# Kernel tuning notes

Hardware: AMD Instinct MI355X
Metric: run time of the kernel (lower is better)

The kernel has to match this reference:

```python
import jax, jax.numpy as jnp
import numpy as np

B, T, D = 32, 512, 1024
P, E, K = 512, 256, 14
NH, L, FF, TOPK = 4, 2, 2048, 7
FOLD_DIV = 2
EPS = 1e-5


def _ln(x, g, b):
    m = x.mean(-1, keepdims=True)
    v = ((x - m) ** 2).mean(-1, keepdims=True)
    return (x - m) * jax.lax.rsqrt(v + EPS) * g + b


def _bn(x, g, b, m, v):  # eval-mode BatchNorm1d with running stats
    return (x - m) * jax.lax.rsqrt(v + EPS) * g + b


def _attn(q, k, v, nh):
    Bq, Tq, Eq = q.shape
    Tk = k.shape[1]
    hd = Eq // nh
    qh = q.reshape(Bq, Tq, nh, hd).transpose(0, 2, 1, 3)
    kh = k.reshape(Bq, Tk, nh, hd).transpose(0, 2, 1, 3)
    vh = v.reshape(Bq, Tk, nh, hd).transpose(0, 2, 1, 3)
    s = jnp.einsum('bhqd,bhkd->bhqk', qh, kh) / jnp.sqrt(jnp.float32(hd))
    a = jax.nn.softmax(s, axis=-1)
    o = jnp.einsum('bhqk,bhkd->bhqd', a, vh)
    return o.transpose(0, 2, 1, 3).reshape(Bq, Tq, Eq)


def setup_inputs() -> dict:
    key = jax.random.key(0)
    ks = iter(jax.random.split(key, 64))

    def rn(shape, s=0.02):
        return jax.random.normal(next(ks), shape, jnp.float32) * s

    return dict(
        x=jax.random.normal(next(ks), (B, T, D), jnp.float32),
        pred_w=rn((D,)), pred_b=jnp.zeros(()),
        t_wqkv=rn((L, D, 3 * D)), t_bqkv=jnp.zeros((L, 3 * D)),
        t_wo=rn((L, D, D)), t_bo=jnp.zeros((L, D)),
        t_ln1g=jnp.ones((L, D)), t_ln1b=jnp.zeros((L, D)),
        t_w1=rn((L, D, FF)), t_b1=jnp.zeros((L, FF)),
        t_w2=rn((L, FF, D)), t_b2=jnp.zeros((L, D)),
        t_ln2g=jnp.ones((L, D)), t_ln2b=jnp.zeros((L, D)),
        sb_w=rn((D, P)), sb_b=jnp.zeros((P,)),
        bn1_g=jnp.ones((P,)), bn1_b=jnp.zeros((P,)), bn1_m=jnp.zeros((P,)), bn1_v=jnp.ones((P,)),
        dt_w=rn((P,)), dt_b=jnp.zeros(()),
        cc_w1=rn((P, 256)), cc_b1=jnp.zeros((256,)),
        bn2_g=jnp.ones((256,)), bn2_b=jnp.zeros((256,)), bn2_m=jnp.zeros((256,)), bn2_v=jnp.ones((256,)),
        cc_w2=rn((256, K)), cc_b2=jnp.zeros((K,)),
        ce=rn((K, E), 1.0),
        kp_w=rn((P, E)), kp_b=jnp.zeros((E,)),
        ca_wqkv=rn((E, 3 * E)), ca_bqkv=jnp.zeros((3 * E,)),
        ca_wo=rn((E, E)), ca_bo=jnp.zeros((E,)),
        fp_w=rn((E, D)), fp_b=jnp.zeros((D,)),
        df_w=rn((P,)), df_b=jnp.zeros(()),
    )


def reference(x, pred_w, pred_b, t_wqkv, t_bqkv, t_wo, t_bo, t_ln1g, t_ln1b, t_w1, t_b1,
              t_w2, t_b2, t_ln2g, t_ln2b, sb_w, sb_b, bn1_g, bn1_b, bn1_m, bn1_v,
              dt_w, dt_b, cc_w1, cc_b1, bn2_g, bn2_b, bn2_m, bn2_v, cc_w2, cc_b2,
              ce, kp_w, kp_b, ca_wqkv, ca_bqkv, ca_wo, ca_bo, fp_w, fp_b, df_w, df_b):
    # --- GlobalAdaptiveTSM: per-token adaptive channel shift, fully vectorized ---
    ratio = jax.nn.sigmoid(jnp.einsum('btd,d->bt', x, pred_w) + pred_b)  # ShiftPredictor
    fold = D // FOLD_DIV
    sn = (ratio * fold).astype(jnp.int32)[..., None]                     # [B,T,1]
    z = jnp.zeros_like(x[:, :1])
    x_prev = jnp.concatenate([z, x[:, :-1]], axis=1)   # t=0 region stays zero
    x_next = jnp.concatenate([x[:, 1:], z], axis=1)    # t=T-1 region stays zero
    c = jnp.arange(D)
    h = jnp.where(c < sn, x_prev, jnp.where(c < 2 * sn, x_next, x))
    # --- TemporalTransformer: 2 post-norm encoder layers (eval mode) ---
    for l in range(L):
        qkv = h @ t_wqkv[l] + t_bqkv[l]
        q, k, v = jnp.split(qkv, 3, axis=-1)
        a = _attn(q, k, v, NH) @ t_wo[l] + t_bo[l]
        h = _ln(h + a, t_ln1g[l], t_ln1b[l])
        f = jax.nn.relu(h @ t_w1[l] + t_b1[l]) @ t_w2[l] + t_b2[l]
        h = _ln(h + f, t_ln2g[l], t_ln2b[l])

    def backbone(zz):
        return jax.nn.relu(_bn(zz @ sb_w + sb_b, bn1_g, bn1_b, bn1_m, bn1_v))

    shared = backbone(h)                                      # [B,T,P]
    top_scores = jnp.einsum('btp,p->bt', shared, dt_w) + dt_b
    _, idx = jax.lax.top_k(top_scores, TOPK)
    agg = jnp.take_along_axis(shared, idx[..., None], axis=1).mean(1)  # [B,P]
    c1 = jax.nn.relu(_bn(agg @ cc_w1 + cc_b1, bn2_g, bn2_b, bn2_m, bn2_v))
    logits = c1 @ cc_w2 + cc_b2                               # [B,K]
    cat_emb = jax.nn.softmax(logits, axis=-1) @ ce            # [B,E]
    proj = shared @ kp_w + kp_b                               # [B,T,E]
    q = cat_emb[:, None, :] @ ca_wqkv[:, :E] + ca_bqkv[:E]
    k = proj @ ca_wqkv[:, E:2 * E] + ca_bqkv[E:2 * E]
    v = proj @ ca_wqkv[:, 2 * E:] + ca_bqkv[2 * E:]
    ctx = _attn(q, k, v, NH) @ ca_wo + ca_bo                  # [B,1,E] broadcasts over T
    final = proj + ctx
    fin_proj = backbone(final @ fp_w + fp_b)
    seg = jnp.einsum('btp,p->bt', fin_proj, df_w) + df_b
    return seg, logits
```

## Files before the change

### kernel.cpp

```cpp
#include <hip/hip_runtime.h>
#include <math.h>

#define Bz 32
#define Tz 512
#define Dz 1024
#define Pz 512
#define Ez 256
#define KC 14
#define NHz 4
#define Lz 2
#define FFz 2048
#define TOPKz 7
#define EPSz 1e-5f
#define BT (Bz*Tz)

typedef unsigned short ushort_t;
typedef __attribute__((ext_vector_type(8))) short short8;
typedef __attribute__((ext_vector_type(4))) float f32x4;

__device__ __forceinline__ ushort_t f2bf(float f) {
    union { float f; unsigned int u; } x; x.f = f;
    unsigned int r = x.u + 0x7fffu + ((x.u >> 16) & 1u);
    return (ushort_t)(r >> 16);
}
__device__ __forceinline__ float bf2f(ushort_t h) {
    union { unsigned int u; float f; } x; x.u = ((unsigned int)h) << 16; return x.f;
}

__global__ __launch_bounds__(256) void mgemm_k(
    const ushort_t* __restrict__ A, int lda,
    const ushort_t* __restrict__ Wt,
    const float* __restrict__ bias,
    float* __restrict__ Cf, ushort_t* __restrict__ Ch, int ldc,
    int Kd, int epi,
    const float* __restrict__ bng, const float* __restrict__ bnb,
    const float* __restrict__ bnm, const float* __restrict__ bnv)
{
    __shared__ __align__(16) ushort_t As[128 * 32];
    __shared__ __align__(16) ushort_t Bs[128 * 32];
    const int tid = threadIdx.x;
    const int lane = tid & 63, wid = tid >> 6;
    const int row0 = blockIdx.y * 128, col0 = blockIdx.x * 128;
    const int wrow = (wid >> 1) * 64, wcol = (wid & 1) * 64;
    const int srow = (lane >> 2);
    const int skoff = (lane & 3) * 8;

    f32x4 acc[4][4];
    const f32x4 zr = {0.f, 0.f, 0.f, 0.f};
    #pragma unroll
    for (int m = 0; m < 4; m++)
        #pragma unroll
        for (int n = 0; n < 4; n++) acc[m][n] = zr;

    for (int k0 = 0; k0 < Kd; k0 += 32) {
        #pragma unroll
        for (int j = 0; j < 2; j++) {
            const int r = wid * 32 + j * 16;
            const ushort_t* ga = A + (size_t)(row0 + r + srow) * lda + k0 + skoff;
            __builtin_amdgcn_global_load_lds(
                (const __attribute__((address_space(1))) unsigned int*)ga,
                (__attribute__((address_space(3))) unsigned int*)(As + r * 32), 16, 0, 0);
            const ushort_t* gb = Wt + (size_t)(col0 + r + srow) * Kd + k0 + skoff;
            __builtin_amdgcn_global_load_lds(
                (const __attribute__((address_space(1))) unsigned int*)gb,
                (__attribute__((address_space(3))) unsigned int*)(Bs + r * 32), 16, 0, 0);
        }
        __syncthreads();
        short8 af[4], bf[4];
        #pragma unroll
        for (int m = 0; m < 4; m++)
            af[m] = *(const short8*)(As + (wrow + m * 16 + (lane & 15)) * 32 + (lane >> 4) * 8);
        #pragma unroll
        for (int n = 0; n < 4; n++)
            bf[n] = *(const short8*)(Bs + (wcol + n * 16 + (lane & 15)) * 32 + (lane >> 4) * 8);
        #pragma unroll
        for (int m = 0; m < 4; m++)
            #pragma unroll
            for (int n = 0; n < 4; n++)
                acc[m][n] = __builtin_amdgcn_mfma_f32_16x16x32_bf16(af[m], bf[n], acc[m][n], 0, 0, 0);
        __syncthreads();
    }

    #pragma unroll
    for (int n = 0; n < 4; n++) {
        const int ccol = col0 + wcol + n * 16 + (lane & 15);
        const float bb = bias[ccol];
        float bsc = 1.f, bsh = 0.f;
        if (epi == 2) {
            bsc = rsqrtf(bnv[ccol] + EPSz) * bng[ccol];
            bsh = bnb[ccol] - bnm[ccol] * bsc;
        }
        #pragma unroll
        for (int m = 0; m < 4; m++) {
            #pragma unroll
            for (int r = 0; r < 4; r++) {
                const int crow = row0 + wrow + m * 16 + (lane >> 4) * 4 + r;
                float y = acc[m][n][r] + bb;
                if (epi == 2) y = y * bsc + bsh;
                if (epi >= 1) y = fmaxf(y, 0.f);
                if (Cf) Cf[(size_t)crow * ldc + ccol] = y;
                if (Ch) Ch[(size_t)crow * ldc + ccol] = f2bf(y);
            }
        }
    }
}

__global__ __launch_bounds__(256) void bgemm_k(
    const ushort_t* __restrict__ A0, int lda, size_t Abz, int Ahz,
    const ushort_t* __restrict__ W0, int ldw, size_t Wbz, int Whz,
    float* __restrict__ Cf0, ushort_t* __restrict__ Ch0, int ldc, size_t Cbz, int Chz, int Kd)
{
    const int z = blockIdx.z, bl = z >> 2, hh = z & 3;
    const ushort_t* A = A0 + (size_t)bl * Abz + (size_t)hh * Ahz;
    const ushort_t* W = W0 + (size_t)bl * Wbz + (size_t)hh * Whz;

    __shared__ __align__(16) ushort_t As[128 * 32];
    __shared__ __align__(16) ushort_t Bs[128 * 32];
    const int tid = threadIdx.x;
    const int lane = tid & 63, wid = tid >> 6;
    const int row0 = blockIdx.y * 128, col0 = blockIdx.x * 128;
    const int wrow = (wid >> 1) * 64, wcol = (wid & 1) * 64;
    const int srow = (lane >> 2);
    const int skoff = (lane & 3) * 8;

    f32x4 acc[4][4];
    const f32x4 zr = {0.f, 0.f, 0.f, 0.f};
    #pragma unroll
    for (int m = 0; m < 4; m++)
        #pragma unroll
        for (int n = 0; n < 4; n++) acc[m][n] = zr;

    for (int k0 = 0; k0 < Kd; k0 += 32) {
        #pragma unroll
        for (int j = 0; j < 2; j++) {
            const int r = wid * 32 + j * 16;
            const ushort_t* ga = A + (size_t)(row0 + r + srow) * lda + k0 + skoff;
            __builtin_amdgcn_global_load_lds(
                (const __attribute__((address_space(1))) unsigned int*)ga,
                (__attribute__((address_space(3))) unsigned int*)(As + r * 32), 16, 0, 0);
            const ushort_t* gb = W + (size_t)(col0 + r + srow) * ldw + k0 + skoff;
            __builtin_amdgcn_global_load_lds(
                (const __attribute__((address_space(1))) unsigned int*)gb,
                (__attribute__((address_space(3))) unsigned int*)(Bs + r * 32), 16, 0, 0);
        }
        __syncthreads();
        short8 af[4], bf[4];
        #pragma unroll
        for (int m = 0; m < 4; m++)
            af[m] = *(const short8*)(As + (wrow + m * 16 + (lane & 15)) * 32 + (lane >> 4) * 8);
        #pragma unroll
        for (int n = 0; n < 4; n++)
            bf[n] = *(const short8*)(Bs + (wcol + n * 16 + (lane & 15)) * 32 + (lane >> 4) * 8);
        #pragma unroll
        for (int m = 0; m < 4; m++)
            #pragma unroll
            for (int n = 0; n < 4; n++)
                acc[m][n] = __builtin_amdgcn_mfma_f32_16x16x32_bf16(af[m], bf[n], acc[m][n], 0, 0, 0);
        __syncthreads();
    }

    #pragma unroll
    for (int n = 0; n < 4; n++) {
        const int ccol = col0 + wcol + n * 16 + (lane & 15);
        #pragma unroll
        for (int m = 0; m < 4; m++) {
            #pragma unroll
            for (int r = 0; r < 4; r++) {
                const int crow = row0 + wrow + m * 16 + (lane >> 4) * 4 + r;
                const float y = acc[m][n][r];
                if (Cf0) (Cf0 + (size_t)bl * Cbz + (size_t)hh * Chz)[(size_t)crow * ldc + ccol] = y;
                if (Ch0) (Ch0 + (size_t)bl * Cbz + (size_t)hh * Chz)[(size_t)crow * ldc + ccol] = f2bf(y);
            }
        }
    }
}

__global__ __launch_bounds__(256) void softmax_k(ushort_t* __restrict__ SP)
{
    const int row = blockIdx.x * 4 + (threadIdx.x >> 6);
    const int lane = threadIdx.x & 63;
    ushort_t* rp = SP + (size_t)row * 512 + lane * 8;
    union { ushort_t h[8]; uint4 u; } in;
    in.u = *(const uint4*)rp;
    float v[8];
    #pragma unroll
    for (int i = 0; i < 8; i++) v[i] = bf2f(in.h[i]) * 0.0625f;
    float m = v[0];
    #pragma unroll
    for (int i = 1; i < 8; i++) m = fmaxf(m, v[i]);
    #pragma unroll
    for (int off = 32; off > 0; off >>= 1) m = fmaxf(m, __shfl_xor(m, off));
    float s = 0.f;
    #pragma unroll
    for (int i = 0; i < 8; i++) { v[i] = expf(v[i] - m); s += v[i]; }
    #pragma unroll
    for (int off = 32; off > 0; off >>= 1) s += __shfl_xor(s, off);
    const float inv = 1.f / s;
    union { ushort_t h[8]; uint4 u; } pk;
    #pragma unroll
    for (int i = 0; i < 8; i++) pk.h[i] = f2bf(v[i] * inv);
    *(uint4*)rp = pk.u;
}

__global__ __launch_bounds__(256) void vtb_k(
    const ushort_t* __restrict__ qkvb, ushort_t* __restrict__ Vt)
{
    const int z = blockIdx.z, bl = z >> 2, hh = z & 3;
    const ushort_t* src = qkvb + (size_t)bl * 512 * 3072 + 2048 + hh * 256;
    ushort_t* dst = Vt + (size_t)z * 256 * 512;
    __shared__ ushort_t t[32][33];
    const int tx = threadIdx.x & 31, ty = threadIdx.x >> 5;
    const int gx = blockIdx.x * 32;
    const int gy = blockIdx.y * 32;
    #pragma unroll
    for (int i = 0; i < 4; i++) {
        const int row = ty + i * 8;
        t[row][tx] = src[(size_t)(gy + row) * 3072 + gx + tx];
    }
    __syncthreads();
    #pragma unroll
    for (int i = 0; i < 4; i++) {
        const int nr = ty + i * 8;
        dst[(size_t)(gx + nr) * 512 + gy + tx] = t[tx][nr];
    }
}

struct WtJobs {
    const float* src[13];
    ushort_t*    dst[13];
    int ld[13];
    int Kd[13];
    int nx[13];
    int base[14];
};

__global__ __launch_bounds__(256) void wtall_k(WtJobs J)
{
    const int bid = blockIdx.x;
    int j = 0;
    #pragma unroll
    for (int i = 0; i < 12; i++) if (bid >= J.base[i + 1]) j = i + 1;
    const int local = bid - J.base[j];
    const int bx = local % J.nx[j], by = local / J.nx[j];
    const float* src = J.src[j];
    ushort_t* dst = J.dst[j];
    const int ld = J.ld[j], Kd = J.Kd[j];

    __shared__ float t[32][33];
    const int tx = threadIdx.x & 31, ty = threadIdx.x >> 5;
    const int gx = bx * 32;
    const int gy = by * 32;
    #pragma unroll
    for (int i = 0; i < 4; i++) {
        const int row = ty + i * 8;
        t[row][tx] = src[(size_t)(gy + row) * ld + gx + tx];
    }
    __syncthreads();
    #pragma unroll
    for (int i = 0; i < 4; i++) {
        const int nr = ty + i * 8;
        dst[(size_t)(gx + nr) * Kd + gy + tx] = f2bf(t[tx][nr]);
    }
}

__global__ __launch_bounds__(256) void predshift_k(
    const float* __restrict__ x, const float* __restrict__ pred_w,
    const float* __restrict__ pred_b, ushort_t* __restrict__ hb)
{
    const int row = blockIdx.x, tid = threadIdx.x;
    const size_t base = (size_t)row * Dz;
    float s = 0.f;
    #pragma unroll
    for (int i = 0; i < 4; i++) {
        int c = tid + i * 256;
        s += x[base + c] * pred_w[c];
    }
    __shared__ float red[256];
    __shared__ int sns;
    red[tid] = s; __syncthreads();
    for (int off = 128; off > 0; off >>= 1) {
        if (tid < off) red[tid] += red[tid + off];
        __syncthreads();
    }
    if (tid == 0) {
        float sg = 1.f / (1.f + expf(-(red[0] + pred_b[0])));
        sns = (int)(sg * (float)(Dz / 2));
    }
    __syncthreads();
    const int sn = sns;
    const int t = row & (Tz - 1);
    #pragma unroll
    for (int i = 0; i < 4; i++) {
        const int c = tid + i * 256;
        const size_t idx = base + c;
        float v;
        if (c < sn)          v = (t > 0)      ? x[idx - Dz] : 0.f;
        else if (c < 2 * sn) v = (t < Tz - 1) ? x[idx + Dz] : 0.f;
        else                 v = x[idx];
        hb[idx] = f2bf(v);
    }
}

__global__ __launch_bounds__(256) void addlnb_k(
    ushort_t* __restrict__ hb, const ushort_t* __restrict__ r,
    const float* __restrict__ g, const float* __restrict__ b)
{
    const int row = blockIdx.x, tid = threadIdx.x;
    const size_t base = (size_t)row * Dz;
    float x[4]; float s = 0.f, sq = 0.f;
    #pragma unroll
    for (int i = 0; i < 4; i++) {
        const int c = tid + i * 256;
        x[i] = bf2f(hb[base + c]) + bf2f(r[base + c]);
        s += x[i]; sq += x[i] * x[i];
    }
    __shared__ float rs[256], rq[256];
    rs[tid] = s; rq[tid] = sq; __syncthreads();
    for (int off = 128; off > 0; off >>= 1) {
        if (tid < off) { rs[tid] += rs[tid + off]; rq[tid] += rq[tid + off]; }
        __syncthreads();
    }
    float mean = rs[0] * (1.f / Dz);
    float var = rq[0] * (1.f / Dz) - mean * mean;
    float inv = rsqrtf(var + EPSz);
    #pragma unroll
    for (int i = 0; i < 4; i++) {
        int c = tid + i * 256;
        float y = (x[i] - mean) * inv * g[c] + b[c];
        hb[base + c] = f2bf(y);
    }
}

__global__ __launch_bounds__(256) void rowdot_k(
    const float* __restrict__ in, const float* __restrict__ w,
    const float* __restrict__ bptr, float* __restrict__ outf)
{
    const int row = blockIdx.x, tid = threadIdx.x;
    const float* r = in + (size_t)row * Pz;
    float s = 0.f;
    #pragma unroll
    for (int c = tid; c < Pz; c += 256) s += r[c] * w[c];
    __shared__ float red[256];
    red[tid] = s; __syncthreads();
    for (int off = 128; off > 0; off >>= 1) {
        if (tid < off) red[tid] += red[tid + off];
        __syncthreads();
    }
    if (tid == 0) outf[row] = red[0] + bptr[0];
}

__global__ __launch_bounds__(256) void topk_k(const float* __restrict__ scores, int* __restrict__ idx)
{
    const int b = blockIdx.x, tid = threadIdx.x;
    __shared__ float sv[Tz];
    __shared__ float rv[256]; __shared__ int ri[256];
    sv[tid] = scores[b * Tz + tid];
    sv[tid + 256] = scores[b * Tz + tid + 256];
    __syncthreads();
    for (int it = 0; it < TOPKz; it++) {
        float v0 = sv[tid]; int i0 = tid;
        float v1 = sv[tid + 256];
        if (v1 > v0) { v0 = v1; i0 = tid + 256; }
        rv[tid] = v0; ri[tid] = i0; __syncthreads();
        for (int off = 128; off > 0; off >>= 1) {
            if (tid < off) {
                if (rv[tid + off] > rv[tid] ||
                    (rv[tid + off] == rv[tid] && ri[tid + off] < ri[tid])) {
                    rv[tid] = rv[tid + off]; ri[tid] = ri[tid + off];
                }
            }
            __syncthreads();
        }
        if (tid == 0) { idx[b * TOPKz + it] = ri[0]; sv[ri[0]] = -INFINITY; }
        __syncthreads();
    }
}

__global__ __launch_bounds__(256) void agg_k(
    const float* __restrict__ sh, const int* __restrict__ idx, float* __restrict__ agg)
{
    const int b = blockIdx.x, tid = threadIdx.x;
    for (int p = tid; p < Pz; p += 256) {
        float s = 0.f;
        #pragma unroll
        for (int j = 0; j < TOPKz; j++) {
            int t = idx[b * TOPKz + j];
            s += sh[((size_t)b * Tz + t) * Pz + p];
        }
        agg[b * Pz + p] = s * (1.f / TOPKz);
    }
}

__global__ __launch_bounds__(256) void cls_k(
    const float* __restrict__ agg,
    const float* __restrict__ cc_w1, const float* __restrict__ cc_b1,
    const float* __restrict__ g2, const float* __restrict__ b2,
    const float* __restrict__ m2, const float* __restrict__ v2,
    const float* __restrict__ cc_w2, const float* __restrict__ cc_b2,
    const float* __restrict__ ce,
    const float* __restrict__ ca_wqkv, const float* __restrict__ ca_bqkv,
    float* __restrict__ logits_out, float* __restrict__ qx)
{
    const int b = blockIdx.x, tid = threadIdx.x;
    __shared__ float ag[Pz], c1s[256], sm[16], cemb[256];
    ag[tid] = agg[b * Pz + tid];
    ag[tid + 256] = agg[b * Pz + tid + 256];
    __syncthreads();
    float s = 0.f;
    for (int p = 0; p < Pz; p++) s += ag[p] * cc_w1[p * 256 + tid];
    s += cc_b1[tid];
    s = (s - m2[tid]) * rsqrtf(v2[tid] + EPSz) * g2[tid] + b2[tid];
    s = fmaxf(s, 0.f);
    c1s[tid] = s;
    __syncthreads();
    if (tid < KC) {
        float l = 0.f;
        for (int e = 0; e < 256; e++) l += c1s[e] * cc_w2[e * KC + tid];
        l += cc_b2[tid];
        sm[tid] = l;
        logits_out[b * KC + tid] = l;
    }
    __syncthreads();
    if (tid == 0) {
        float mx = sm[0];
        for (int k = 1; k < KC; k++) mx = fmaxf(mx, sm[k]);
        float su = 0.f;
        for (int k = 0; k < KC; k++) { sm[k] = expf(sm[k] - mx); su += sm[k]; }
        float inv = 1.f / su;
        for (int k = 0; k < KC; k++) sm[k] *= inv;
    }
    __syncthreads();
    float cesum = 0.f;
    #pragma unroll
    for (int k = 0; k < KC; k++) cesum += sm[k] * ce[k * 256 + tid];
    cemb[tid] = cesum; __syncthreads();
    float q = 0.f;
    for (int i = 0; i < 256; i++) q += cemb[i] * ca_wqkv[i * 768 + tid];
    qx[b * 256 + tid] = q + ca_bqkv[tid];
}

__global__ __launch_bounds__(256) void xattn_k(
    const float* __restrict__ qx, const float* __restrict__ kv,
    const float* __restrict__ ca_wo, const float* __restrict__ ca_bo,
    float* __restrict__ ctx2)
{
    const int b = blockIdx.x, tid = threadIdx.x;
    __shared__ float q4[256];
    __shared__ float sc[NHz][Tz];
    __shared__ float cx[256];
    q4[tid] = qx[b * 256 + tid];
    __syncthreads();
    for (int si = tid; si < NHz * Tz; si += 256) {
        int hh = si >> 9, t = si & (Tz - 1);
        const float* kr = kv + ((size_t)b * Tz + t) * 512 + hh * 64;
        const float* qr = q4 + hh * 64;
        float s = 0.f;
        #pragma unroll 8
        for (int d = 0; d < 64; d++) s += qr[d] * kr[d];
        sc[hh][t] = s * 0.125f;
    }
    __syncthreads();
    const int hh = tid >> 6, lane = tid & 63;
    float mx = -INFINITY;
    for (int t = lane; t < Tz; t += 64) mx = fmaxf(mx, sc[hh][t]);
    for (int off = 32; off > 0; off >>= 1) mx = fmaxf(mx, __shfl_xor(mx, off));
    float su = 0.f;
    for (int t = lane; t < Tz; t += 64) { float e = expf(sc[hh][t] - mx); sc[hh][t] = e; su += e; }
    for (int off = 32; off > 0; off >>= 1) su += __shfl_xor(su, off);
    float inv = 1.f / su;
    __syncthreads();
    float acc = 0.f;
    for (int t = 0; t < Tz; t++) acc += sc[hh][t] * kv[((size_t)b * Tz + t) * 512 + 256 + tid];
    cx[tid] = acc * inv;
    __syncthreads();
    float s2 = 0.f;
    for (int i = 0; i < 256; i++) s2 += cx[i] * ca_wo[i * 256 + tid];
    ctx2[b * 256 + tid] = s2 + ca_bo[tid];
}

__global__ __launch_bounds__(256) void addctx_k(
    const float* __restrict__ proj, const float* __restrict__ ctx2, ushort_t* __restrict__ fb)
{
    size_t idx = (size_t)blockIdx.x * 256 + threadIdx.x;
    int e = (int)(idx & 255);
    int b = (int)(idx >> 17);
    fb[idx] = f2bf(proj[idx] + ctx2[b * 256 + e]);
}

extern "C" void kernel_launch(void* const* d_in, const int* in_sizes, int n_in,
                              void* d_out, int out_size, void* d_ws, size_t ws_size,
                              hipStream_t stream)
{
    const float* x       = (const float*)d_in[0];
    const float* pred_w  = (const float*)d_in[1];
    const float* pred_b  = (const float*)d_in[2];
    const float* t_wqkv  = (const float*)d_in[3];
    const float* t_bqkv  = (const float*)d_in[4];
    const float* t_wo    = (const float*)d_in[5];
    const float* t_bo    = (const float*)d_in[6];
    const float* t_ln1g  = (const float*)d_in[7];
    const float* t_ln1b  = (const float*)d_in[8];
    const float* t_w1    = (const float*)d_in[9];
    const float* t_b1    = (const float*)d_in[10];
    const float* t_w2    = (const float*)d_in[11];
    const float* t_b2    = (const float*)d_in[12];
    const float* t_ln2g  = (const float*)d_in[13];
    const float* t_ln2b  = (const float*)d_in[14];
    const float* sb_w    = (const float*)d_in[15];
    const float* sb_b    = (const float*)d_in[16];
    const float* bn1_g   = (const float*)d_in[17];
    const float* bn1_b   = (const float*)d_in[18];
    const float* bn1_m   = (const float*)d_in[19];
    const float* bn1_v   = (const float*)d_in[20];
    const float* dt_w    = (const float*)d_in[21];
    const float* dt_b    = (const float*)d_in[22];
    const float* cc_w1   = (const float*)d_in[23];
    const float* cc_b1   = (const float*)d_in[24];
    const float* bn2_g   = (const float*)d_in[25];
    const float* bn2_b   = (const float*)d_in[26];
    const float* bn2_m   = (const float*)d_in[27];
    const float* bn2_v   = (const float*)d_in[28];
    const float* cc_w2   = (const float*)d_in[29];
    const float* cc_b2   = (const float*)d_in[30];
    const float* ce      = (const float*)d_in[31];
    const float* kp_w    = (const float*)d_in[32];
    const float* kp_b    = (const float*)d_in[33];
    const float* ca_wqkv = (const float*)d_in[34];
    const float* ca_bqkv = (const float*)d_in[35];
    const float* ca_wo   = (const float*)d_in[36];
    const float* ca_bo   = (const float*)d_in[37];
    const float* fp_w    = (const float*)d_in[38];
    const float* fp_b    = (const float*)d_in[39];
    const float* df_w    = (const float*)d_in[40];
    const float* df_b    = (const float*)d_in[41];

    float* out = (float*)d_out;

    char* wp = (char*)d_ws;
    auto alloc = [&](size_t bytes) -> char* {
        char* r = wp; wp += (bytes + 255) & ~(size_t)255; return r;
    };
    float* scores  = (float*)alloc(BT * 4);
    int*   tkidx   = (int*)alloc(256 * 4);
    float* aggbuf  = (float*)alloc((size_t)Bz * Pz * 4);
    float* qxbuf   = (float*)alloc((size_t)Bz * Ez * 4);
    float* ctx2buf = (float*)alloc((size_t)Bz * Ez * 4);

    const size_t WT_TOTAL = 2*(size_t)3072*1024 + 2*(size_t)1024*1024 + 2*(size_t)2048*1024
                          + 2*(size_t)1024*2048 + (size_t)512*1024 + (size_t)256*512
                          + 2*(size_t)256*256 + (size_t)1024*256;
    ushort_t* wtb = (ushort_t*)alloc(WT_TOTAL * 2);
    size_t woff = 0;
    auto nxt = [&](size_t n) -> ushort_t* { ushort_t* r = wtb + woff; woff += n; return r; };
    ushort_t* qkvT[2] = { nxt((size_t)3072*1024), nxt((size_t)3072*1024) };
    ushort_t* woT[2]  = { nxt((size_t)1024*1024), nxt((size_t)1024*1024) };
    ushort_t* w1T[2]  = { nxt((size_t)2048*1024), nxt((size_t)2048*1024) };
    ushort_t* w2T[2]  = { nxt((size_t)1024*2048), nxt((size_t)1024*2048) };
    ushort_t* sbT  = nxt((size_t)512*1024);
    ushort_t* kpT  = nxt((size_t)256*512);
    ushort_t* kvT  = nxt((size_t)512*256);
    ushort_t* fpT  = nxt((size_t)1024*256);

    size_t fixedB = (size_t)(wp - (char*)d_ws);
    int Bc = Bz;
    while (Bc > 1 && fixedB + (size_t)Bc * Tz * 22528 + 1048576 > ws_size) Bc >>= 1;
    const int Rmax = Bc * Tz;
    ushort_t* hb   = (ushort_t*)alloc((size_t)Rmax * 1024 * 2);
    ushort_t* qkvb = (ushort_t*)alloc((size_t)Rmax * 3072 * 2);
    float*    scr  = (float*)alloc((size_t)Rmax * 2048 * 4);
    ushort_t* Pb   = (ushort_t*)alloc((size_t)Rmax * 2048 * 2);
    ushort_t* Vt   = (ushort_t*)alloc((size_t)Rmax * 1024 * 2);

    {
        WtJobs J;
        const float* srcs[13] = { t_wqkv, t_wqkv + (size_t)1024*3072, t_wo, t_wo + (size_t)1024*1024,
                                  t_w1, t_w1 + (size_t)1024*2048, t_w2, t_w2 + (size_t)2048*1024,
                                  sb_w, kp_w, ca_wqkv + Ez, ca_wqkv + 2*Ez, fp_w };
        ushort_t* dsts[13] = { qkvT[0], qkvT[1], woT[0], woT[1], w1T[0], w1T[1], w2T[0], w2T[1],
                               sbT, kpT, kvT, kvT + (size_t)256*256, fpT };
        const int lds_[13] = { 3072, 3072, 1024, 1024, 2048, 2048, 1024, 1024, 512, 256, 768, 768, 1024 };
        const int kds_[13] = { 1024, 1024, 1024, 1024, 1024, 1024, 2048, 2048, 1024, 512, 256, 256, 256 };
        const int nxs_[13] = { 96, 96, 32, 32, 64, 64, 32, 32, 16, 8, 8, 8, 32 };
        const int nys_[13] = { 32, 32, 32, 32, 32, 32, 64, 64, 32, 16, 8, 8, 8 };
        int acc = 0;
        for (int i = 0; i < 13; i++) {
            J.src[i] = srcs[i]; J.dst[i] = dsts[i];
            J.ld[i] = lds_[i]; J.Kd[i] = kds_[i]; J.nx[i] = nxs_[i];
            J.base[i] = acc; acc += nxs_[i] * nys_[i];
        }
        J.base[13] = acc;
        wtall_k<<<acc, 256, 0, stream>>>(J);
    }

    for (int b0 = 0; b0 < Bz; b0 += Bc) {
        const int R = Bc * Tz;
        const float* xc = x + (size_t)b0 * Tz * Dz;

        auto MG = [&](const ushort_t* Ain, int lda, const ushort_t* Wt_, const float* bias,
                      float* Cf, ushort_t* Ch, int ldc, int N, int Kd, int epi,
                      const float* g = nullptr, const float* bb = nullptr,
                      const float* m = nullptr, const float* v = nullptr) {
            mgemm_k<<<dim3(N/128, R/128), 256, 0, stream>>>(
                Ain, lda, Wt_, bias, Cf, Ch, ldc, Kd, epi, g, bb, m, v);
        };

        predshift_k<<<R, 256, 0, stream>>>(xc, pred_w, pred_b, hb);

        for (int l = 0; l < Lz; l++) {
            MG(hb, 1024, qkvT[l], t_bqkv + (size_t)l*3072, nullptr, qkvb, 3072, 3072, 1024, 0);
            vtb_k<<<dim3(8, 16, Bc * 4), 256, 0, stream>>>(qkvb, Vt);
            bgemm_k<<<dim3(4, 4, Bc * 4), 256, 0, stream>>>(
                qkvb, 3072, (size_t)512 * 3072, 256,
                qkvb + 1024, 3072, (size_t)512 * 3072, 256,
                nullptr, Pb, 512, (size_t)4 * 512 * 512, 512 * 512, 256);
            softmax_k<<<R, 256, 0, stream>>>(Pb);
            bgemm_k<<<dim3(2, 4, Bc * 4), 256, 0, stream>>>(
                Pb, 512, (size_t)4 * 512 * 512, 512 * 512,
                Vt, 512, (size_t)4 * 256 * 512, 256 * 512,
                nullptr, qkvb, 3072, (size_t)512 * 3072, 256, 512);
            MG(qkvb, 3072, woT[l], t_bo + (size_t)l*1024, nullptr, Pb, 1024, 1024, 1024, 0);
            addlnb_k<<<R, 256, 0, stream>>>(hb, Pb,
                                            t_ln1g + (size_t)l*Dz, t_ln1b + (size_t)l*Dz);
            MG(hb, 1024, w1T[l], t_b1 + (size_t)l*FFz, nullptr, qkvb, 2048, 2048, 1024, 1);
            MG(qkvb, 2048, w2T[l], t_b2 + (size_t)l*Dz, nullptr, Pb, 1024, 1024, 2048, 0);
            addlnb_k<<<R, 256, 0, stream>>>(hb, Pb,
                                            t_ln2g + (size_t)l*Dz, t_ln2b + (size_t)l*Dz);
        }

        float*    shared  = scr;
        float*    proj    = scr + (size_t)R * 512;
        float*    kvb     = scr + (size_t)R * 768;
        float*    fin     = scr + (size_t)R * 1280;
        ushort_t* sharedb = Pb;
        ushort_t* projb   = Pb + (size_t)R * 512;
        ushort_t* fb      = Pb + (size_t)R * 768;
        ushort_t* fpb     = qkvb;

        MG(hb, 1024, sbT, sb_b, shared, sharedb, 512, 512, 1024, 2, bn1_g, bn1_b, bn1_m, bn1_v);
        rowdot_k<<<R, 256, 0, stream>>>(shared, dt_w, dt_b, scores + (size_t)b0 * Tz);
        topk_k<<<Bc, 256, 0, stream>>>(scores + (size_t)b0 * Tz, tkidx);
        agg_k<<<Bc, 256, 0, stream>>>(shared, tkidx, aggbuf);
        cls_k<<<Bc, 256, 0, stream>>>(aggbuf, cc_w1, cc_b1, bn2_g, bn2_b, bn2_m, bn2_v,
                                      cc_w2, cc_b2, ce, ca_wqkv, ca_bqkv,
                                      out + BT + (size_t)b0 * KC, qxbuf);
        MG(sharedb, 512, kpT, kp_b, proj, projb, 256, 256, 512, 0);
        MG(projb, 256, kvT, ca_bqkv + Ez, kvb, nullptr, 512, 512, 256, 0);
        xattn_k<<<Bc, 256, 0, stream>>>(qxbuf, kvb, ca_wo, ca_bo, ctx2buf);
        addctx_k<<<(R * Ez) / 256, 256, 0, stream>>>(proj, ctx2buf, fb);
        MG(fb, 256, fpT, fp_b, nullptr, fpb, 1024, 1024, 256, 0);
        MG(fpb, 1024, sbT, sb_b, fin, nullptr, 512, 512, 1024, 2, bn1_g, bn1_b, bn1_m, bn1_v);
        rowdot_k<<<R, 256, 0, stream>>>(fin, df_w, df_b, out + (size_t)b0 * Tz);
    }
}
```

Before: 1.804 ms.

## Fuse QK^T with V transpose, fuse score/topk/agg/classifier, reuse buffers

Merges the V-transpose kernel and the QK^T batched GEMM into one launch whose blocks split between the two jobs. It also folds the row-dot score, top-k, gather-mean and classifier into one per-batch kernel. The fp32 scratch buffer is dropped and its tensors are aliased onto existing bf16 buffers, which lowers the workspace need per batch chunk so larger chunks may fit. The intent is fewer launches and less intermediate traffic. The cost is that the score row-dot now runs with only one block per batch, which gives low parallelism over 512x512 floats per batch.

```diff
diff --git a/kernel.cpp b/kernel.cpp
--- a/kernel.cpp
+++ b/kernel.cpp
@@ -175,6 +175,96 @@
     }
 }
 
+__global__ __launch_bounds__(256) void qkvt_k(
+    const ushort_t* __restrict__ qkvb, ushort_t* __restrict__ Sb, ushort_t* __restrict__ Vt)
+{
+    __shared__ __align__(16) ushort_t smem[2][128 * 32];
+    const int bx = blockIdx.x, z = blockIdx.y;
+    const int bl = z >> 2, hh = z & 3;
+    const int tid = threadIdx.x;
+
+    if (bx < 16) {
+        const ushort_t* A = qkvb + (size_t)bl * 512 * 3072 + hh * 256;
+        const ushort_t* W = qkvb + (size_t)bl * 512 * 3072 + 1024 + hh * 256;
+        ushort_t* C = Sb + (size_t)z * 512 * 512;
+        ushort_t* As = smem[0];
+        ushort_t* Bs = smem[1];
+        const int lane = tid & 63, wid = tid >> 6;
+        const int row0 = (bx >> 2) * 128, col0 = (bx & 3) * 128;
+        const int wrow = (wid >> 1) * 64, wcol = (wid & 1) * 64;
+        const int srow = (lane >> 2);
+        const int skoff = (lane & 3) * 8;
+
+        f32x4 acc[4][4];
+        const f32x4 zr = {0.f, 0.f, 0.f, 0.f};
+        #pragma unroll
+        for (int m = 0; m < 4; m++)
+            #pragma unroll
+            for (int n = 0; n < 4; n++) acc[m][n] = zr;
+
+        for (int k0 = 0; k0 < 256; k0 += 32) {
+            #pragma unroll
+            for (int j = 0; j < 2; j++) {
+                const int r = wid * 32 + j * 16;
+                const ushort_t* ga = A + (size_t)(row0 + r + srow) * 3072 + k0 + skoff;
+                __builtin_amdgcn_global_load_lds(
+                    (const __attribute__((address_space(1))) unsigned int*)ga,
+                    (__attribute__((address_space(3))) unsigned int*)(As + r * 32), 16, 0, 0);
+                const ushort_t* gb = W + (size_t)(col0 + r + srow) * 3072 + k0 + skoff;
+                __builtin_amdgcn_global_load_lds(
+                    (const __attribute__((address_space(1))) unsigned int*)gb,
+                    (__attribute__((address_space(3))) unsigned int*)(Bs + r * 32), 16, 0, 0);
+            }
+            __syncthreads();
+            short8 af[4], bf[4];
+            #pragma unroll
+            for (int m = 0; m < 4; m++)
+                af[m] = *(const short8*)(As + (wrow + m * 16 + (lane & 15)) * 32 + (lane >> 4) * 8);
+            #pragma unroll
+            for (int n = 0; n < 4; n++)
+                bf[n] = *(const short8*)(Bs + (wcol + n * 16 + (lane & 15)) * 32 + (lane >> 4) * 8);
+            #pragma unroll
+            for (int m = 0; m < 4; m++)
+                #pragma unroll
+                for (int n = 0; n < 4; n++)
+                    acc[m][n] = __builtin_amdgcn_mfma_f32_16x16x32_bf16(af[m], bf[n], acc[m][n], 0, 0, 0);
+            __syncthreads();
+        }
+
+        #pragma unroll
+        for (int n = 0; n < 4; n++) {
+            const int ccol = col0 + wcol + n * 16 + (lane & 15);
+            #pragma unroll
+            for (int m = 0; m < 4; m++) {
+                #pragma unroll
+                for (int r = 0; r < 4; r++) {
+                    const int crow = row0 + wrow + m * 16 + (lane >> 4) * 4 + r;
+                    C[(size_t)crow * 512 + ccol] = f2bf(acc[m][n][r]);
+                }
+            }
+        }
+    } else {
+        const int local = bx - 16;
+        const int gx = (local & 7) * 32;
+        const int gy = (local >> 3) * 32;
+        const ushort_t* src = qkvb + (size_t)bl * 512 * 3072 + 2048 + hh * 256;
+        ushort_t* dst = Vt + (size_t)z * 256 * 512;
+        ushort_t (*t)[33] = (ushort_t(*)[33])smem;
+        const int tx = tid & 31, ty = tid >> 5;
+        #pragma unroll
+        for (int i = 0; i < 4; i++) {
+            const int row = ty + i * 8;
+            t[row][tx] = src[(size_t)(gy + row) * 3072 + gx + tx];
+        }
+        __syncthreads();
+        #pragma unroll
+        for (int i = 0; i < 4; i++) {
+            const int nr = ty + i * 8;
+            dst[(size_t)(gx + nr) * 512 + gy + tx] = t[tx][nr];
+        }
+    }
+}
+
 __global__ __launch_bounds__(256) void softmax_k(ushort_t* __restrict__ SP)
 {
     const int row = blockIdx.x * 4 + (threadIdx.x >> 6);
@@ -200,29 +290,6 @@
     #pragma unroll
     for (int i = 0; i < 8; i++) pk.h[i] = f2bf(v[i] * inv);
     *(uint4*)rp = pk.u;
-}
-
-__global__ __launch_bounds__(256) void vtb_k(
-    const ushort_t* __restrict__ qkvb, ushort_t* __restrict__ Vt)
-{
-    const int z = blockIdx.z, bl = z >> 2, hh = z & 3;
-    const ushort_t* src = qkvb + (size_t)bl * 512 * 3072 + 2048 + hh * 256;
-    ushort_t* dst = Vt + (size_t)z * 256 * 512;
-    __shared__ ushort_t t[32][33];
-    const int tx = threadIdx.x & 31, ty = threadIdx.x >> 5;
-    const int gx = blockIdx.x * 32;
-    const int gy = blockIdx.y * 32;
-    #pragma unroll
-    for (int i = 0; i < 4; i++) {
-        const int row = ty + i * 8;
-        t[row][tx] = src[(size_t)(gy + row) * 3072 + gx + tx];
-    }
-    __syncthreads();
-    #pragma unroll
-    for (int i = 0; i < 4; i++) {
-        const int nr = ty + i * 8;
-        dst[(size_t)(gx + nr) * 512 + gy + tx] = t[tx][nr];
-    }
 }
 
 struct WtJobs {
@@ -349,14 +416,42 @@
     if (tid == 0) outf[row] = red[0] + bptr[0];
 }
 
-__global__ __launch_bounds__(256) void topk_k(const float* __restrict__ scores, int* __restrict__ idx)
+__global__ __launch_bounds__(256) void clsfused_k(
+    const float* __restrict__ shared_, const float* __restrict__ dt_w, const float* __restrict__ dt_b,
+    const float* __restrict__ cc_w1, const float* __restrict__ cc_b1,
+    const float* __restrict__ g2, const float* __restrict__ b2,
+    const float* __restrict__ m2, const float* __restrict__ v2,
+    const float* __restrict__ cc_w2, const float* __restrict__ cc_b2,
+    const float* __restrict__ ce,
+    const float* __restrict__ ca_wqkv, const float* __restrict__ ca_bqkv,
+    float* __restrict__ logits_out, float* __restrict__ qx)
 {
     const int b = blockIdx.x, tid = threadIdx.x;
     __shared__ float sv[Tz];
+    __shared__ float dw[Pz];
     __shared__ float rv[256]; __shared__ int ri[256];
-    sv[tid] = scores[b * Tz + tid];
-    sv[tid + 256] = scores[b * Tz + tid + 256];
-    __syncthreads();
+    __shared__ int tki[TOPKz];
+    __shared__ float ag[Pz], c1s[256], sm[16], cemb[256];
+
+    dw[tid] = dt_w[tid]; dw[tid + 256] = dt_w[tid + 256];
+    __syncthreads();
+
+    const float* base = shared_ + (size_t)b * Tz * Pz;
+    const float db = dt_b[0];
+    const int wv = tid >> 6, lane = tid & 63;
+    for (int r = wv; r < Tz; r += 4) {
+        const float* row = base + (size_t)r * Pz + lane * 8;
+        const float4 a0 = *(const float4*)row;
+        const float4 a1 = *(const float4*)(row + 4);
+        const int c0 = lane * 8;
+        float s = a0.x * dw[c0] + a0.y * dw[c0 + 1] + a0.z * dw[c0 + 2] + a0.w * dw[c0 + 3]
+                + a1.x * dw[c0 + 4] + a1.y * dw[c0 + 5] + a1.z * dw[c0 + 6] + a1.w * dw[c0 + 7];
+        #pragma unroll
+        for (int off = 32; off > 0; off >>= 1) s += __shfl_xor(s, off);
+        if (lane == 0) sv[r] = s + db;
+    }
+    __syncthreads();
+
     for (int it = 0; it < TOPKz; it++) {
         float v0 = sv[tid]; int i0 = tid;
         float v1 = sv[tid + 256];
@@ -371,41 +466,18 @@
             }
             __syncthreads();
         }
-        if (tid == 0) { idx[b * TOPKz + it] = ri[0]; sv[ri[0]] = -INFINITY; }
-        __syncthreads();
-    }
-}
-
-__global__ __launch_bounds__(256) void agg_k(
-    const float* __restrict__ sh, const int* __restrict__ idx, float* __restrict__ agg)
-{
-    const int b = blockIdx.x, tid = threadIdx.x;
+        if (tid == 0) { tki[it] = ri[0]; sv[ri[0]] = -INFINITY; }
+        __syncthreads();
+    }
+
     for (int p = tid; p < Pz; p += 256) {
         float s = 0.f;
         #pragma unroll
-        for (int j = 0; j < TOPKz; j++) {
-            int t = idx[b * TOPKz + j];
-            s += sh[((size_t)b * Tz + t) * Pz + p];
-        }
-        agg[b * Pz + p] = s * (1.f / TOPKz);
-    }
-}
-
-__global__ __launch_bounds__(256) void cls_k(
-    const float* __restrict__ agg,
-    const float* __restrict__ cc_w1, const float* __restrict__ cc_b1,
-    const float* __restrict__ g2, const float* __restrict__ b2,
-    const float* __restrict__ m2, const float* __restrict__ v2,
-    const float* __restrict__ cc_w2, const float* __restrict__ cc_b2,
-    const float* __restrict__ ce,
-    const float* __restrict__ ca_wqkv, const float* __restrict__ ca_bqkv,
-    float* __restrict__ logits_out, float* __restrict__ qx)
-{
-    const int b = blockIdx.x, tid = threadIdx.x;
-    __shared__ float ag[Pz], c1s[256], sm[16], cemb[256];
-    ag[tid] = agg[b * Pz + tid];
-    ag[tid + 256] = agg[b * Pz + tid + 256];
-    __syncthreads();
+        for (int j = 0; j < TOPKz; j++) s += base[(size_t)tki[j] * Pz + p];
+        ag[p] = s * (1.f / TOPKz);
+    }
+    __syncthreads();
+
     float s = 0.f;
     for (int p = 0; p < Pz; p++) s += ag[p] * cc_w1[p * 256 + tid];
     s += cc_b1[tid];
@@ -540,9 +612,6 @@
     auto alloc = [&](size_t bytes) -> char* {
         char* r = wp; wp += (bytes + 255) & ~(size_t)255; return r;
     };
-    float* scores  = (float*)alloc(BT * 4);
-    int*   tkidx   = (int*)alloc(256 * 4);
-    float* aggbuf  = (float*)alloc((size_t)Bz * Pz * 4);
     float* qxbuf   = (float*)alloc((size_t)Bz * Ez * 4);
     float* ctx2buf = (float*)alloc((size_t)Bz * Ez * 4);
 
@@ -563,11 +632,10 @@
 
     size_t fixedB = (size_t)(wp - (char*)d_ws);
     int Bc = Bz;
-    while (Bc > 1 && fixedB + (size_t)Bc * Tz * 22528 + 1048576 > ws_size) Bc >>= 1;
+    while (Bc > 1 && fixedB + (size_t)Bc * Tz * 14336 + 1048576 > ws_size) Bc >>= 1;
     const int Rmax = Bc * Tz;
     ushort_t* hb   = (ushort_t*)alloc((size_t)Rmax * 1024 * 2);
     ushort_t* qkvb = (ushort_t*)alloc((size_t)Rmax * 3072 * 2);
-    float*    scr  = (float*)alloc((size_t)Rmax * 2048 * 4);
     ushort_t* Pb   = (ushort_t*)alloc((size_t)Rmax * 2048 * 2);
     ushort_t* Vt   = (ushort_t*)alloc((size_t)Rmax * 1024 * 2);
 
@@ -608,11 +676,7 @@
 
         for (int l = 0; l < Lz; l++) {
             MG(hb, 1024, qkvT[l], t_bqkv + (size_t)l*3072, nullptr, qkvb, 3072, 3072, 1024, 0);
-            vtb_k<<<dim3(8, 16, Bc * 4), 256, 0, stream>>>(qkvb, Vt);
-            bgemm_k<<<dim3(4, 4, Bc * 4), 256, 0, stream>>>(
-                qkvb, 3072, (size_t)512 * 3072, 256,
-                qkvb + 1024, 3072, (size_t)512 * 3072, 256,
-                nullptr, Pb, 512, (size_t)4 * 512 * 512, 512 * 512, 256);
+            qkvt_k<<<dim3(144, Bc * 4), 256, 0, stream>>>(qkvb, Pb, Vt);
             softmax_k<<<R, 256, 0, stream>>>(Pb);
             bgemm_k<<<dim3(2, 4, Bc * 4), 256, 0, stream>>>(
                 Pb, 512, (size_t)4 * 512 * 512, 512 * 512,
@@ -627,22 +691,20 @@
                                             t_ln2g + (size_t)l*Dz, t_ln2b + (size_t)l*Dz);
         }
 
-        float*    shared  = scr;
-        float*    proj    = scr + (size_t)R * 512;
-        float*    kvb     = scr + (size_t)R * 768;
-        float*    fin     = scr + (size_t)R * 1280;
+        float*    shared  = (float*)Vt;
+        float*    proj    = (float*)hb;
+        float*    kvb     = (float*)(qkvb + (size_t)R * 1024);
+        float*    fin     = (float*)(Pb + (size_t)R * 1024);
         ushort_t* sharedb = Pb;
         ushort_t* projb   = Pb + (size_t)R * 512;
         ushort_t* fb      = Pb + (size_t)R * 768;
         ushort_t* fpb     = qkvb;
 
         MG(hb, 1024, sbT, sb_b, shared, sharedb, 512, 512, 1024, 2, bn1_g, bn1_b, bn1_m, bn1_v);
-        rowdot_k<<<R, 256, 0, stream>>>(shared, dt_w, dt_b, scores + (size_t)b0 * Tz);
-        topk_k<<<Bc, 256, 0, stream>>>(scores + (size_t)b0 * Tz, tkidx);
-        agg_k<<<Bc, 256, 0, stream>>>(shared, tkidx, aggbuf);
-        cls_k<<<Bc, 256, 0, stream>>>(aggbuf, cc_w1, cc_b1, bn2_g, bn2_b, bn2_m, bn2_v,
-                                      cc_w2, cc_b2, ce, ca_wqkv, ca_bqkv,
-                                      out + BT + (size_t)b0 * KC, qxbuf);
+        clsfused_k<<<Bc, 256, 0, stream>>>(shared, dt_w, dt_b, cc_w1, cc_b1,
+                                           bn2_g, bn2_b, bn2_m, bn2_v, cc_w2, cc_b2,
+                                           ce, ca_wqkv, ca_bqkv,
+                                           out + BT + (size_t)b0 * KC, qxbuf);
         MG(sharedb, 512, kpT, kp_b, proj, projb, 256, 256, 512, 0);
         MG(projb, 256, kvT, ca_bqkv + Ez, kvb, nullptr, 512, 512, 256, 0);
         xattn_k<<<Bc, 256, 0, stream>>>(qxbuf, kvb, ca_wo, ca_bo, ctx2buf);
```

Result: slower. 1.853 ms (+2.8%).
